# Optimization experiments

Hardware: AMD Instinct MI355X
Metric: run time of the kernel (lower is better)

The kernel has to match this reference:

```python
import jax, jax.numpy as jnp
import numpy as np

UNITS = 100000      # output nodes (len(adjlist))
N_IN = 100000       # input nodes
DEGREE = 16         # neighbors per output node
E = UNITS * DEGREE  # total edges = num_edges_adjlist
B = 16              # batch
F = 4               # input features


def setup_inputs() -> dict:
    key = jax.random.key(0)
    k_x, k_w, k_b, k_src = jax.random.split(key, 4)
    x = jax.random.normal(k_x, (B, N_IN, F), dtype=jnp.float32)
    # Per-edge learned scale and bias (share_weights=True, use_bias=True)
    kernel = jax.random.normal(k_w, (E,), dtype=jnp.float32)
    bias = jax.random.normal(k_b, (E,), dtype=jnp.float32)
    # Flattened adjlist: src_idx[e] = input node gathered for edge e (jlist),
    # seg_ids[e] = output node receiving edge e (ilist) -> repeat(arange(UNITS), DEGREE)
    src_idx = jax.random.randint(k_src, (E,), 0, N_IN, dtype=jnp.int32)
    seg_ids = jnp.repeat(jnp.arange(UNITS, dtype=jnp.int32), DEGREE)
    return {"x": x, "kernel": kernel, "bias": bias,
            "src_idx": src_idx, "seg_ids": seg_ids}


def reference(x, kernel, bias, src_idx, seg_ids):
    # Original: for each feature i, flat_f = adjmat @ x[:,:,i].T  (edge gather),
    #   flat_f2 = flat_f * kernel + bias, f_out = reshapemat @ flat_f2.T (segment sum).
    # Vectorized over features since weights are shared (share_weights=True).
    gathered = x[:, src_idx, :]                              # [B, E, F]
    edge_vals = gathered * kernel[None, :, None] + bias[None, :, None]
    # segment-sum over edges into output nodes
    out = jax.ops.segment_sum(edge_vals.transpose(1, 0, 2),  # [E, B, F]
                              seg_ids, num_segments=UNITS)   # [UNITS, B, F]
    out = out.transpose(1, 0, 2)                             # [B, UNITS, F]
    return out  # activation=None -> linear
```

## Files before the change

### kernel.cpp

```cpp
#include <hip/hip_runtime.h>
#include <hip/hip_bf16.h>

#define UNITS  100000
#define N_IN   100000
#define DEGREE 16
#define NB     16
#define NF     4

typedef float          f32x4 __attribute__((ext_vector_type(4)));
typedef unsigned short u16x8 __attribute__((ext_vector_type(8)));

__device__ __forceinline__ float bf2f(unsigned short u) {
    return __uint_as_float((unsigned)u << 16);
}

__global__ __launch_bounds__(256) void conv_transpose(
    const float4* __restrict__ x,
    ushort4*      __restrict__ xh)
{
    __shared__ ushort4 tile[256][17];
    const int tid = (int)threadIdx.x;
    const int s0  = (int)blockIdx.x * 256;

#pragma unroll
    for (int b = 0; b < NB; ++b) {
        int s = s0 + tid;
        if (s < N_IN) {
            float4 v = x[(size_t)b * N_IN + s];
            ushort4 h;
            h.x = __bfloat16_as_ushort(__float2bfloat16(v.x));
            h.y = __bfloat16_as_ushort(__float2bfloat16(v.y));
            h.z = __bfloat16_as_ushort(__float2bfloat16(v.z));
            h.w = __bfloat16_as_ushort(__float2bfloat16(v.w));
            tile[tid][b] = h;
        }
    }
    __syncthreads();
#pragma unroll
    for (int i = 0; i < 16; ++i) {
        int idx = i * 256 + tid;
        int sl  = idx >> 4;
        int b   = idx & 15;
        int s   = s0 + sl;
        if (s < N_IN) xh[(size_t)s * NB + b] = tile[sl][b];
    }
}

__global__ __launch_bounds__(256) void pc_main_h2(
    const unsigned short* __restrict__ xh,
    const float*  __restrict__ kern,
    const float*  __restrict__ bias,
    const int*    __restrict__ src,
    float*        __restrict__ out)
{
    __shared__ int   s_sh[32 * 17];
    __shared__ float k_sh[32 * 17];
    __shared__ float bsum_sh[32];
    __shared__ f32x4 o_sh[16][33];

    const int tid = (int)threadIdx.x;
    const int u0  = (int)blockIdx.x * 32;
    const int e0  = u0 * DEGREE;

#pragma unroll
    for (int h = 0; h < 2; ++h) {
        int idx = h * 256 + tid;
        int e   = e0 + idx;
        int ul  = idx >> 4;
        int d   = idx & 15;
        s_sh[ul * 17 + d] = __builtin_nontemporal_load(src + e);
        k_sh[ul * 17 + d] = __builtin_nontemporal_load(kern + e);
        float bv = __builtin_nontemporal_load(bias + e);
        for (int off = 8; off; off >>= 1) bv += __shfl_down(bv, off, 16);
        if (d == 0) bsum_sh[ul] = bv;
    }
    __syncthreads();

    const int ul = tid >> 3;
    const int p  = tid & 7;

    f32x4 a0 = {0.f, 0.f, 0.f, 0.f};
    f32x4 a1 = {0.f, 0.f, 0.f, 0.f};
#pragma unroll
    for (int d = 0; d < DEGREE; ++d) {
        int   s = s_sh[ul * 17 + d];
        float k = k_sh[ul * 17 + d];
        u16x8 v = *(const u16x8*)(xh + (size_t)s * 64 + p * 8);
        a0.x = fmaf(k, bf2f(v[0]), a0.x);
        a0.y = fmaf(k, bf2f(v[1]), a0.y);
        a0.z = fmaf(k, bf2f(v[2]), a0.z);
        a0.w = fmaf(k, bf2f(v[3]), a0.w);
        a1.x = fmaf(k, bf2f(v[4]), a1.x);
        a1.y = fmaf(k, bf2f(v[5]), a1.y);
        a1.z = fmaf(k, bf2f(v[6]), a1.z);
        a1.w = fmaf(k, bf2f(v[7]), a1.w);
    }
    const float bs = bsum_sh[ul];
    a0.x += bs; a0.y += bs; a0.z += bs; a0.w += bs;
    a1.x += bs; a1.y += bs; a1.z += bs; a1.w += bs;

    o_sh[2 * p + 0][ul] = a0;
    o_sh[2 * p + 1][ul] = a1;
    __syncthreads();

#pragma unroll
    for (int j = 0; j < 2; ++j) {
        int idx = j * 256 + tid;
        int b   = idx >> 5;
        int u   = idx & 31;
        f32x4 val = o_sh[b][u];
        f32x4* optr = (f32x4*)(out + ((size_t)b * UNITS + (u0 + u)) * NF);
        __builtin_nontemporal_store(val, optr);
    }
}

__global__ __launch_bounds__(256) void pc_fallback(
    const float* __restrict__ x, const float* __restrict__ kern,
    const float* __restrict__ bias, const int* __restrict__ src,
    float* __restrict__ out)
{
    const int UBLK = (UNITS + 255) / 256;
    int bid  = (int)blockIdx.x;
    int b_lo = bid & 7;
    int grp  = bid >> 3;
    int b    = b_lo + ((grp >= UBLK) ? 8 : 0);
    int ublk = (grp >= UBLK) ? (grp - UBLK) : grp;
    int u    = ublk * 256 + (int)threadIdx.x;
    if (u >= UNITS) return;
    const int e0 = u * DEGREE;
    int sidx[DEGREE]; float kv[DEGREE]; float bsum = 0.0f;
#pragma unroll
    for (int q = 0; q < 4; ++q) {
        int4   s  = *(const int4*)  (src  + e0 + q * 4);
        float4 k  = *(const float4*)(kern + e0 + q * 4);
        float4 bb = *(const float4*)(bias + e0 + q * 4);
        sidx[q*4+0]=s.x; kv[q*4+0]=k.x; sidx[q*4+1]=s.y; kv[q*4+1]=k.y;
        sidx[q*4+2]=s.z; kv[q*4+2]=k.z; sidx[q*4+3]=s.w; kv[q*4+3]=k.w;
        bsum += bb.x + bb.y + bb.z + bb.w;
    }
    const float* xb = x + (size_t)b * N_IN * NF;
    float4 acc = make_float4(bsum, bsum, bsum, bsum);
#pragma unroll
    for (int d = 0; d < DEGREE; ++d) {
        float4 xv = *(const float4*)(xb + (size_t)sidx[d] * NF);
        acc.x += kv[d]*xv.x; acc.y += kv[d]*xv.y;
        acc.z += kv[d]*xv.z; acc.w += kv[d]*xv.w;
    }
    *(float4*)(out + ((size_t)b * UNITS + u) * NF) = acc;
}

extern "C" void kernel_launch(void* const* d_in, const int* in_sizes, int n_in,
                              void* d_out, int out_size, void* d_ws, size_t ws_size,
                              hipStream_t stream) {
    const float* x    = (const float*)d_in[0];
    const float* kern = (const float*)d_in[1];
    const float* bias = (const float*)d_in[2];
    const int*   src  = (const int*)d_in[3];
    float* out = (float*)d_out;

    const size_t xh_bytes = (size_t)N_IN * NB * NF * sizeof(unsigned short);
    if (ws_size >= xh_bytes) {
        ushort4* xh = (ushort4*)d_ws;
        conv_transpose<<<(N_IN + 255) / 256, 256, 0, stream>>>(
            (const float4*)x, xh);
        pc_main_h2<<<UNITS / 32, 256, 0, stream>>>(
            (const unsigned short*)xh, kern, bias, src, out);
    } else {
        const int UBLK = (UNITS + 255) / 256;
        pc_fallback<<<NB * UBLK, 256, 0, stream>>>(x, kern, bias, src, out);
    }
}
```

Measured before the change: 42.06 us.

## Partition batch into XCC-affine groups with per-group bf16 x copies

Splits the batch into 4 groups of 4, lays out the bf16 x copy per group (32 bytes per node), and has each block claim a tile through per-group atomic counters selected by its XCC ID. This is meant to keep each group's gather working set (3.2 MB) resident in the L2 of the XCCs that serve it. A prep kernel also converts kernel weights to bf16 and precomputes per-unit bias sums, so the main kernel loads less per edge. The costs are that src indices and weights are reloaded once per group (4x), the atomic claim adds latency at block start, and storing the weights in bf16 adds rounding error.

```diff
diff --git a/kernel.cpp b/kernel.cpp
--- a/kernel.cpp
+++ b/kernel.cpp
@@ -6,6 +6,13 @@
 #define DEGREE 16
 #define NB     16
 #define NF     4
+#define E_TOT  (UNITS * DEGREE)
+
+#define G           4
+#define BPG         (NB / G)
+#define TU          128
+#define TILES_PER_G ((UNITS + TU - 1) / TU)
+#define NBLK        (G * TILES_PER_G)
 
 typedef float          f32x4 __attribute__((ext_vector_type(4)));
 typedef unsigned short u16x8 __attribute__((ext_vector_type(8)));
@@ -14,14 +21,171 @@
     return __uint_as_float((unsigned)u << 16);
 }
 
+#define XH_OFF   0u
+#define KH_OFF   12800000u
+#define BS_OFF   16000000u
+#define CNT_OFF  16400000u
+#define WS_NEED  (16400000u + 16u)
+
+__global__ __launch_bounds__(256) void prep(
+    const float4* __restrict__ x,
+    const float*  __restrict__ kern,
+    const float*  __restrict__ bias,
+    ushort4*       __restrict__ xh,
+    unsigned short* __restrict__ kh,
+    float*         __restrict__ bsum,
+    int*           __restrict__ cnt)
+{
+    __shared__ ushort4 tile[256][17];
+    const int bid = (int)blockIdx.x;
+    const int tid = (int)threadIdx.x;
+    if (bid == 0 && tid < G) cnt[tid] = 0;
+
+    if (bid < 391) {
+        const int s0 = bid * 256;
+#pragma unroll
+        for (int b = 0; b < NB; ++b) {
+            int s = s0 + tid;
+            if (s < N_IN) {
+                float4 v = x[(size_t)b * N_IN + s];
+                ushort4 h;
+                h.x = __bfloat16_as_ushort(__float2bfloat16(v.x));
+                h.y = __bfloat16_as_ushort(__float2bfloat16(v.y));
+                h.z = __bfloat16_as_ushort(__float2bfloat16(v.z));
+                h.w = __bfloat16_as_ushort(__float2bfloat16(v.w));
+                tile[tid][b] = h;
+            }
+        }
+        __syncthreads();
+#pragma unroll
+        for (int j = 0; j < 16; ++j) {
+            int idx = j * 256 + tid;
+            int sl  = idx >> 4;
+            int b   = idx & 15;
+            int s   = s0 + sl;
+            if (s < N_IN) {
+                int g = b >> 2, bl = b & 3;
+                xh[((size_t)g * N_IN + s) * BPG + bl] = tile[sl][b];
+            }
+        }
+    } else if (bid < 391 + 782) {
+        int base = (bid - 391) * 2048 + tid * 8;
+        if (base < E_TOT) {
+            float4 a = *(const float4*)(kern + base);
+            float4 b4 = *(const float4*)(kern + base + 4);
+            u16x8 h;
+            h[0] = __bfloat16_as_ushort(__float2bfloat16(a.x));
+            h[1] = __bfloat16_as_ushort(__float2bfloat16(a.y));
+            h[2] = __bfloat16_as_ushort(__float2bfloat16(a.z));
+            h[3] = __bfloat16_as_ushort(__float2bfloat16(a.w));
+            h[4] = __bfloat16_as_ushort(__float2bfloat16(b4.x));
+            h[5] = __bfloat16_as_ushort(__float2bfloat16(b4.y));
+            h[6] = __bfloat16_as_ushort(__float2bfloat16(b4.z));
+            h[7] = __bfloat16_as_ushort(__float2bfloat16(b4.w));
+            *(u16x8*)(kh + base) = h;
+        }
+    } else {
+        int u = (bid - 1173) * 256 + tid;
+        if (u < UNITS) {
+            const float4* bp = (const float4*)(bias + (size_t)u * DEGREE);
+            float4 b0 = bp[0], b1 = bp[1], b2 = bp[2], b3 = bp[3];
+            float s01 = ((b0.x + b0.y) + (b0.z + b0.w)) +
+                        ((b1.x + b1.y) + (b1.z + b1.w));
+            float s23 = ((b2.x + b2.y) + (b2.z + b2.w)) +
+                        ((b3.x + b3.y) + (b3.z + b3.w));
+            bsum[u] = s01 + s23;
+        }
+    }
+}
+
+__global__ __launch_bounds__(256) void pc_g4(
+    const unsigned short* __restrict__ xh,
+    const unsigned short* __restrict__ kh,
+    const float*          __restrict__ bsum,
+    const int*            __restrict__ src,
+    float*                __restrict__ out,
+    int*                  __restrict__ cnt)
+{
+    __shared__ int   s_sh[TU * 17];
+    __shared__ float k_sh[TU * 17];
+    __shared__ float bs_sh[TU];
+    __shared__ int   claim2[2];
+
+    const int tid = (int)threadIdx.x;
+    if (tid == 0) {
+        unsigned xcc = 0;
+        asm volatile("s_getreg_b32 %0, hwreg(HW_REG_XCC_ID)" : "=s"(xcc));
+        int g = (int)((xcc & 7u) >> 1);
+        int t = atomicAdd(&cnt[g], 1);
+#pragma unroll
+        for (int k = 0; k < G - 1; ++k) {
+            if (t >= TILES_PER_G) { g = (g + 1) & (G - 1); t = atomicAdd(&cnt[g], 1); }
+        }
+        claim2[0] = g; claim2[1] = t;
+    }
+    __syncthreads();
+    const int g    = claim2[0];
+    const int tile = claim2[1];
+    const int u0   = tile * TU;
+    const int e0   = u0 * DEGREE;
+
+#pragma unroll
+    for (int it = 0; it < 8; ++it) {
+        int idx = it * 256 + tid;
+        int ul  = idx >> 4;
+        int sl  = ul * 17 + (idx & 15);
+        if (u0 + ul < UNITS) {
+            s_sh[sl] = __builtin_nontemporal_load(src + e0 + idx);
+            unsigned short kv = __builtin_nontemporal_load(kh + e0 + idx);
+            k_sh[sl] = bf2f(kv);
+        } else { s_sh[sl] = 0; k_sh[sl] = 0.0f; }
+    }
+    if (tid < TU) {
+        int u = u0 + tid;
+        bs_sh[tid] = (u < UNITS) ? bsum[u] : 0.0f;
+    }
+    __syncthreads();
+
+    const int ul = tid >> 1;
+    const int p  = tid & 1;
+    const unsigned short* xg = xh + (size_t)g * N_IN * 16;
+
+    f32x4 a0 = {0.f, 0.f, 0.f, 0.f};
+    f32x4 a1 = {0.f, 0.f, 0.f, 0.f};
+#pragma unroll
+    for (int d = 0; d < DEGREE; ++d) {
+        int   s = s_sh[ul * 17 + d];
+        float k = k_sh[ul * 17 + d];
+        u16x8 v = *(const u16x8*)(xg + (size_t)s * 16 + p * 8);
+        a0.x = fmaf(k, bf2f(v[0]), a0.x);
+        a0.y = fmaf(k, bf2f(v[1]), a0.y);
+        a0.z = fmaf(k, bf2f(v[2]), a0.z);
+        a0.w = fmaf(k, bf2f(v[3]), a0.w);
+        a1.x = fmaf(k, bf2f(v[4]), a1.x);
+        a1.y = fmaf(k, bf2f(v[5]), a1.y);
+        a1.z = fmaf(k, bf2f(v[6]), a1.z);
+        a1.w = fmaf(k, bf2f(v[7]), a1.w);
+    }
+    const float bs = bs_sh[ul];
+    a0 += bs;
+    a1 += bs;
+
+    const int u = u0 + ul;
+    if (u < UNITS) {
+        int b0 = g * BPG + 2 * p;
+        f32x4* o0 = (f32x4*)(out + ((size_t)b0 * UNITS + u) * NF);
+        f32x4* o1 = (f32x4*)(out + ((size_t)(b0 + 1) * UNITS + u) * NF);
+        __builtin_nontemporal_store(a0, o0);
+        __builtin_nontemporal_store(a1, o1);
+    }
+}
+
 __global__ __launch_bounds__(256) void conv_transpose(
-    const float4* __restrict__ x,
-    ushort4*      __restrict__ xh)
+    const float4* __restrict__ x, ushort4* __restrict__ xh)
 {
     __shared__ ushort4 tile[256][17];
     const int tid = (int)threadIdx.x;
     const int s0  = (int)blockIdx.x * 256;
-
 #pragma unroll
     for (int b = 0; b < NB; ++b) {
         int s = s0 + tid;
@@ -47,21 +211,17 @@
 }
 
 __global__ __launch_bounds__(256) void pc_main_h2(
-    const unsigned short* __restrict__ xh,
-    const float*  __restrict__ kern,
-    const float*  __restrict__ bias,
-    const int*    __restrict__ src,
-    float*        __restrict__ out)
+    const unsigned short* __restrict__ xh, const float* __restrict__ kern,
+    const float* __restrict__ bias, const int* __restrict__ src,
+    float* __restrict__ out)
 {
     __shared__ int   s_sh[32 * 17];
     __shared__ float k_sh[32 * 17];
     __shared__ float bsum_sh[32];
     __shared__ f32x4 o_sh[16][33];
-
     const int tid = (int)threadIdx.x;
     const int u0  = (int)blockIdx.x * 32;
     const int e0  = u0 * DEGREE;
-
 #pragma unroll
     for (int h = 0; h < 2; ++h) {
         int idx = h * 256 + tid;
@@ -75,34 +235,24 @@
         if (d == 0) bsum_sh[ul] = bv;
     }
     __syncthreads();
-
     const int ul = tid >> 3;
     const int p  = tid & 7;
-
-    f32x4 a0 = {0.f, 0.f, 0.f, 0.f};
-    f32x4 a1 = {0.f, 0.f, 0.f, 0.f};
+    f32x4 a0 = {0.f,0.f,0.f,0.f}, a1 = {0.f,0.f,0.f,0.f};
 #pragma unroll
     for (int d = 0; d < DEGREE; ++d) {
         int   s = s_sh[ul * 17 + d];
         float k = k_sh[ul * 17 + d];
         u16x8 v = *(const u16x8*)(xh + (size_t)s * 64 + p * 8);
-        a0.x = fmaf(k, bf2f(v[0]), a0.x);
-        a0.y = fmaf(k, bf2f(v[1]), a0.y);
-        a0.z = fmaf(k, bf2f(v[2]), a0.z);
-        a0.w = fmaf(k, bf2f(v[3]), a0.w);
-        a1.x = fmaf(k, bf2f(v[4]), a1.x);
-        a1.y = fmaf(k, bf2f(v[5]), a1.y);
-        a1.z = fmaf(k, bf2f(v[6]), a1.z);
-        a1.w = fmaf(k, bf2f(v[7]), a1.w);
+        a0.x = fmaf(k, bf2f(v[0]), a0.x); a0.y = fmaf(k, bf2f(v[1]), a0.y);
+        a0.z = fmaf(k, bf2f(v[2]), a0.z); a0.w = fmaf(k, bf2f(v[3]), a0.w);
+        a1.x = fmaf(k, bf2f(v[4]), a1.x); a1.y = fmaf(k, bf2f(v[5]), a1.y);
+        a1.z = fmaf(k, bf2f(v[6]), a1.z); a1.w = fmaf(k, bf2f(v[7]), a1.w);
     }
     const float bs = bsum_sh[ul];
-    a0.x += bs; a0.y += bs; a0.z += bs; a0.w += bs;
-    a1.x += bs; a1.y += bs; a1.z += bs; a1.w += bs;
-
-    o_sh[2 * p + 0][ul] = a0;
-    o_sh[2 * p + 1][ul] = a1;
-    __syncthreads();
-
+    a0 += bs; a1 += bs;
+    o_sh[2*p+0][ul] = a0;
+    o_sh[2*p+1][ul] = a1;
+    __syncthreads();
 #pragma unroll
     for (int j = 0; j < 2; ++j) {
         int idx = j * 256 + tid;
@@ -128,7 +278,7 @@
     int u    = ublk * 256 + (int)threadIdx.x;
     if (u >= UNITS) return;
     const int e0 = u * DEGREE;
-    int sidx[DEGREE]; float kv[DEGREE]; float bsum = 0.0f;
+    int sidx[DEGREE]; float kv[DEGREE]; float bsumv = 0.0f;
 #pragma unroll
     for (int q = 0; q < 4; ++q) {
         int4   s  = *(const int4*)  (src  + e0 + q * 4);
@@ -136,10 +286,10 @@
         float4 bb = *(const float4*)(bias + e0 + q * 4);
         sidx[q*4+0]=s.x; kv[q*4+0]=k.x; sidx[q*4+1]=s.y; kv[q*4+1]=k.y;
         sidx[q*4+2]=s.z; kv[q*4+2]=k.z; sidx[q*4+3]=s.w; kv[q*4+3]=k.w;
-        bsum += bb.x + bb.y + bb.z + bb.w;
+        bsumv += bb.x + bb.y + bb.z + bb.w;
     }
     const float* xb = x + (size_t)b * N_IN * NF;
-    float4 acc = make_float4(bsum, bsum, bsum, bsum);
+    float4 acc = make_float4(bsumv, bsumv, bsumv, bsumv);
 #pragma unroll
     for (int d = 0; d < DEGREE; ++d) {
         float4 xv = *(const float4*)(xb + (size_t)sidx[d] * NF);
@@ -157,9 +307,18 @@
     const float* bias = (const float*)d_in[2];
     const int*   src  = (const int*)d_in[3];
     float* out = (float*)d_out;
-
-    const size_t xh_bytes = (size_t)N_IN * NB * NF * sizeof(unsigned short);
-    if (ws_size >= xh_bytes) {
+    char* ws = (char*)d_ws;
+
+    if (ws_size >= WS_NEED) {
+        ushort4*        xh   = (ushort4*)(ws + XH_OFF);
+        unsigned short* kh   = (unsigned short*)(ws + KH_OFF);
+        float*          bsum = (float*)(ws + BS_OFF);
+        int*            cnt  = (int*)(ws + CNT_OFF);
+        prep<<<1564, 256, 0, stream>>>((const float4*)x, kern, bias,
+                                       xh, kh, bsum, cnt);
+        pc_g4<<<NBLK, 256, 0, stream>>>((const unsigned short*)xh, kh, bsum,
+                                        src, out, cnt);
+    } else if (ws_size >= (size_t)N_IN * NB * NF * sizeof(unsigned short)) {
         ushort4* xh = (ushort4*)d_ws;
         conv_transpose<<<(N_IN + 255) / 256, 256, 0, stream>>>(
             (const float4*)x, xh);
```

Measured after the change: 77.27 us. +83.7%, slower.
